# Kernel optimization log

Measured on AMD Instinct MI355X. Metric: run time of the kernel, lower is better.

## Reference

```python
import jax, jax.numpy as jnp
import numpy as np

EPS = 0.05  # mesh.epsilon boundary band


def _pool_one(adj, image, vs, edges):
    # adj: [N,N] bool, image: [N,F] f32, vs: [N,2] f32 in [0,1], edges: [2,E] int32
    N, F = image.shape
    E = edges.shape[1]
    K = N // 2                      # out_target
    tgt_kills = N - K               # number of vertices removed
    v0, v1 = edges[0], edges[1]
    # heap key = sum of squares of concat(image[v0], image[v1])
    cost = jnp.sum(image[v0] * image[v0], -1) + jnp.sum(image[v1] * image[v1], -1)
    def bnd(p):
        return (p[:, 0] < EPS) | (p[:, 0] > 1 - EPS) | (p[:, 1] < EPS) | (p[:, 1] > 1 - EPS)
    ok = ~(bnd(vs[v0]) | bnd(vs[v1]))   # boundary_mask = ~is_boundary
    # heappop of [value, id] lists == stable sort by cost (ties broken by edge id)
    order = jnp.argsort(cost)
    # sequential greedy collapse: kill v1 if edge interior and both endpoints alive
    def step(carry, eid):
        mask, nk = carry
        a, b = v0[eid], v1[eid]
        acc = ok[eid] & mask[a] & mask[b] & (nk < tgt_kills)
        mask = mask.at[b].set(mask[b] & ~acc)
        return (mask, nk + acc.astype(jnp.int32)), acc
    (mask, _), accepts = jax.lax.scan(step, (jnp.ones(N, bool), jnp.int32(0)), order)
    sv0, sv1 = v0[order], v1[order]
    # mapping m: dead vertex -> absorbing vertex (identity elsewhere)
    dead = jnp.where(accepts, sv1, N)          # N = out-of-range -> dropped
    m = jnp.arange(N).at[dead].set(sv0, mode='drop')
    # update_matrix: scatter-add collapsed vertex features into absorber rows
    upd = jnp.zeros_like(image).at[jnp.where(accepts, sv0, N)].add(image[sv1], mode='drop')
    image2 = image + upd
    # merge_vertex on adjacency: union rows then columns of merged vertices
    A = adj.astype(jnp.uint8)
    A1 = jnp.zeros_like(A).at[m].max(A)        # merge rows
    A2 = jnp.zeros_like(A1).at[m].max(A1.T).T  # merge cols
    alive = jnp.nonzero(mask, size=K, fill_value=0)[0]  # exactly K survivors
    adj_out = A2[alive][:, alive].astype(bool) & ~jnp.eye(K, dtype=bool)
    return adj_out, image2[alive]


def setup_inputs() -> dict:
    key = jax.random.key(0)
    k1, k2, k3, k4, k5 = jax.random.split(key, 5)
    B, N, F, E = 4, 8192, 64, 65536
    adj = jax.random.bernoulli(k1, 0.002, (B, N, N))
    image = jax.random.normal(k2, (B, N, F), jnp.float32)
    vs = jax.random.uniform(k3, (B, N, 2), dtype=jnp.float32)
    a = jax.random.randint(k4, (B, 1, E), 0, N)
    off = jax.random.randint(k5, (B, 1, E), 1, N)
    b = (a + off) % N                           # guarantee v0 != v1
    edges = jnp.concatenate([a, b], axis=1).astype(jnp.int32)
    return {"adj": adj, "image": image, "vs": vs, "edges": edges}


def reference(adj, image, vs, edges):
    # returns (pooled adjacency [B,N//2,N//2] bool, pooled features [B,N//2,F])
    return jax.vmap(_pool_one)(adj, image, vs, edges)
```

## Files before the change

kernel.cpp:

```cpp
#include <hip/hip_runtime.h>
#include <stdint.h>

typedef unsigned long long u64;
typedef unsigned int u32;
typedef unsigned char u8;

#define Bn 4
#define Nv 8192
#define Fd 64
#define Ed 65536
#define Kv 4096
#define TGTK 4096
#define NW 256
#define SC 8192

#define SWZ8(i) ((i) ^ (((i) >> 3) & 15))

#define WS_FLAGS   ((size_t)0)
#define WS_ACCCNT  ((size_t)256)
#define WS_OUTBITS ((size_t)512)
#define OUTBITS_BYTES ((size_t)Bn*Kv*128*4)
#define WS_ZERO_BYTES (WS_OUTBITS + OUTBITS_BYTES)
#define WS_KEYS    (WS_ZERO_BYTES)
#define WS_SQ      (WS_KEYS + (size_t)Bn*Ed*8)
#define WS_BND     (WS_SQ + (size_t)Bn*Nv*4)
#define WS_MAP     (WS_BND + (size_t)Bn*Nv)
#define WS_POS     (WS_MAP + (size_t)Bn*Nv*4)
#define WS_PM      (WS_POS + (size_t)Bn*Nv*4)
#define WS_ALIVEW  (WS_PM + (size_t)Bn*Nv*4)
#define WS_ALIST   (WS_ALIVEW + (size_t)Bn*NW*4)
#define WS_ACC     (WS_ALIST + (size_t)Bn*Kv*4)
#define WS_PACK    (WS_ACC + (size_t)Bn*TGTK*2*4)
#define WS_SPACK   (WS_PACK + (size_t)Bn*Ed*4)

__global__ void k_detect(const u8* adj, u32* flags) {
    int tid = blockIdx.x * blockDim.x + threadIdx.x;
    const u32* w = (const u32*)adj;
    bool f0 = false, f1 = false, f2 = false, f3 = false;
    for (int i = tid; i < (1 << 19); i += gridDim.x * blockDim.x) {
        u32 v = w[i];
        f0 |= (v & 0x000000FFu) != 0;
        f1 |= (v & 0x0000FF00u) != 0;
        f2 |= (v & 0x00FF0000u) != 0;
        f3 |= (v & 0xFF000000u) != 0;
    }
    u32 m = 0;
    if (__ballot(f0)) m |= 1;
    if (__ballot(f1)) m |= 2;
    if (__ballot(f2)) m |= 4;
    if (__ballot(f3)) m |= 8;
    if ((threadIdx.x & 63) == 0 && m) atomicOr(flags, m);
}

__global__ void k_vertex(const float* image, const float* vs, float* sq, u8* bnd, int* map) {
#pragma clang fp contract(off)
    int idx = blockIdx.x * 256 + threadIdx.x;
    if (idx >= Bn * Nv) return;
    const float* row = image + (size_t)idx * Fd;
    float r[8];
#pragma unroll
    for (int j = 0; j < 8; ++j) r[j] = row[j] * row[j];
#pragma unroll
    for (int i = 8; i < 64; i += 8)
#pragma unroll
        for (int j = 0; j < 8; ++j) r[j] += row[i + j] * row[i + j];
    float s = ((r[0] + r[1]) + (r[2] + r[3])) + ((r[4] + r[5]) + (r[6] + r[7]));
    sq[idx] = s;
    float x = vs[(size_t)idx * 2], y = vs[(size_t)idx * 2 + 1];
    const float LO = 0.05f;
    const float HI = (float)(1.0 - 0.05);
    bnd[idx] = ((x < LO) || (x > HI) || (y < LO) || (y > HI)) ? 1 : 0;
    map[idx] = idx & (Nv - 1);
}

__global__ void k_edge(const int* edges, const float* sq, const u8* bnd, u64* keys, u32* pack) {
    int idx = blockIdx.x * 256 + threadIdx.x;
    if (idx >= Bn * Ed) return;
    int b = idx >> 16, e = idx & (Ed - 1);
    int v0 = edges[(size_t)b * 2 * Ed + e];
    int v1 = edges[(size_t)b * 2 * Ed + Ed + e];
    float c = sq[b * Nv + v0] + sq[b * Nv + v1];
    keys[idx] = ((u64)__float_as_uint(c) << 16) | (u32)e;
    u32 okk = (!bnd[b * Nv + v0] && !bnd[b * Nv + v1]) ? 1u : 0u;
    pack[idx] = (u32)v0 | ((u32)v1 << 13) | (okk << 26);
}

__device__ __forceinline__ void bitonic_cas(u64* s, int i, int pa, bool asc) {
    u64 a = s[i], c = s[pa];
    if ((a > c) == asc) { s[i] = c; s[pa] = a; }
}
__device__ __forceinline__ void cex(u64& a, u64& b, bool asc) {
    if ((a > b) == asc) { u64 t = a; a = b; b = t; }
}

__global__ __launch_bounds__(1024) void k_sortA(u64* keys) {
    __shared__ u64 s[SC];
    int b = blockIdx.x >> 3, ch = blockIdx.x & 7;
    u64* base = keys + (size_t)b * Ed + (size_t)ch * SC;
    int gb = ch * SC;
    int t8 = threadIdx.x * 8;
    u64 r[8];
#pragma unroll
    for (int u = 0; u < 8; ++u) r[u] = base[t8 + u];
    cex(r[0], r[1], true); cex(r[2], r[3], false); cex(r[4], r[5], true); cex(r[6], r[7], false);
    cex(r[0], r[2], true); cex(r[1], r[3], true); cex(r[4], r[6], false); cex(r[5], r[7], false);
    cex(r[0], r[1], true); cex(r[2], r[3], true); cex(r[4], r[5], false); cex(r[6], r[7], false);
    {
        bool a8 = (((gb + t8) & 8) == 0);
        cex(r[0], r[4], a8); cex(r[1], r[5], a8); cex(r[2], r[6], a8); cex(r[3], r[7], a8);
        cex(r[0], r[2], a8); cex(r[1], r[3], a8); cex(r[4], r[6], a8); cex(r[5], r[7], a8);
        cex(r[0], r[1], a8); cex(r[2], r[3], a8); cex(r[4], r[5], a8); cex(r[6], r[7], a8);
    }
#pragma unroll
    for (int u = 0; u < 8; ++u) s[SWZ8(t8 + u)] = r[u];
    __syncthreads();
    for (int k = 16; k <= SC; k <<= 1) {
        for (int j = k >> 1; j >= 8; j >>= 1) {
#pragma unroll
            for (int p = 0; p < SC / 2048; ++p) {
                int t = p * 1024 + threadIdx.x;
                int i = ((t & ~(j - 1)) << 1) | (t & (j - 1));
                bool asc = (((gb + i) & k) == 0);
                bitonic_cas(s, SWZ8(i), SWZ8(i | j), asc);
            }
            __syncthreads();
        }
        bool asc = (((gb + t8) & k) == 0);
#pragma unroll
        for (int u = 0; u < 8; ++u) r[u] = s[SWZ8(t8 + u)];
        cex(r[0], r[4], asc); cex(r[1], r[5], asc); cex(r[2], r[6], asc); cex(r[3], r[7], asc);
        cex(r[0], r[2], asc); cex(r[1], r[3], asc); cex(r[4], r[6], asc); cex(r[5], r[7], asc);
        cex(r[0], r[1], asc); cex(r[2], r[3], asc); cex(r[4], r[5], asc); cex(r[6], r[7], asc);
        if (k == SC) {
#pragma unroll
            for (int u = 0; u < 8; ++u) base[t8 + u] = r[u];
        } else {
#pragma unroll
            for (int u = 0; u < 8; ++u) s[SWZ8(t8 + u)] = r[u];
            __syncthreads();
        }
    }
}

__global__ void k_sortB(u64* keys, int k, int j) {
    int idx = blockIdx.x * 256 + threadIdx.x;
    if (idx >= Bn * Ed / 2) return;
    int b = idx >> 15, t = idx & (Ed / 2 - 1);
    int i = ((t & ~(j - 1)) << 1) | (t & (j - 1));
    int pa = i | j;
    bool asc = ((i & k) == 0);
    u64* base = keys + (size_t)b * Ed;
    u64 a = base[i], c = base[pa];
    if ((a > c) == asc) { base[i] = c; base[pa] = a; }
}

__global__ __launch_bounds__(1024) void k_sortC(u64* keys, int k,
                                                const u32* pack, u32* spack, int dofin) {
    __shared__ u64 s[SC];
    int b = blockIdx.x >> 3, ch = blockIdx.x & 7;
    u64* base = keys + (size_t)b * Ed + (size_t)ch * SC;
    int gb = ch * SC;
    for (int p = 0; p < SC / 1024; ++p) {
        int i = p * 1024 + threadIdx.x;
        s[SWZ8(i)] = base[i];
    }
    __syncthreads();
    bool asc = ((gb & k) == 0);
    for (int j = SC / 2; j >= 8; j >>= 1) {
#pragma unroll
        for (int p = 0; p < SC / 2048; ++p) {
            int t = p * 1024 + threadIdx.x;
            int i = ((t & ~(j - 1)) << 1) | (t & (j - 1));
            bitonic_cas(s, SWZ8(i), SWZ8(i | j), asc);
        }
        __syncthreads();
    }
    int t8 = threadIdx.x * 8;
    u64 r[8];
#pragma unroll
    for (int u = 0; u < 8; ++u) r[u] = s[SWZ8(t8 + u)];
    cex(r[0], r[4], asc); cex(r[1], r[5], asc); cex(r[2], r[6], asc); cex(r[3], r[7], asc);
    cex(r[0], r[2], asc); cex(r[1], r[3], asc); cex(r[4], r[6], asc); cex(r[5], r[7], asc);
    cex(r[0], r[1], asc); cex(r[2], r[3], asc); cex(r[4], r[5], asc); cex(r[6], r[7], asc);
    if (dofin) {
        const u32* pk = pack + (size_t)b * Ed;
        u32* sp = spack + (size_t)b * Ed + (size_t)ch * SC;
#pragma unroll
        for (int u = 0; u < 8; ++u) sp[t8 + u] = pk[(u32)(r[u] & 0xFFFFu)];
    } else {
#pragma unroll
        for (int u = 0; u < 8; ++u) base[t8 + u] = r[u];
    }
}

__global__ __launch_bounds__(64) void k_greedy(const u32* spack, int* map, u32* aliveW,
                                               int* accList, u32* accCnt) {
    int b = blockIdx.x;
    int lane = threadIdx.x;
    __shared__ u32 alive[NW];
    __shared__ u32 mlane[Nv];
    for (int i = lane; i < NW; i += 64) alive[i] = 0xFFFFFFFFu;
    for (int i = lane; i < Nv; i += 64) mlane[i] = 64u;
    const u32* sp = spack + (size_t)b * Ed;
    u32 pc = sp[lane];
    __syncthreads();
    int nk = 0;
    const int G = Ed / 64;
    for (int g = 0; g < G; ++g) {
        u32 pn = (g + 1 < G) ? sp[(g + 1) * 64 + lane] : 0u;
        int v0 = pc & 8191;
        int v1 = (pc >> 13) & 8191;
        bool okk = (pc >> 26) & 1u;
        bool a0 = (alive[v0 >> 5] >> (v0 & 31)) & 1u;
        bool a1 = (alive[v1 >> 5] >> (v1 & 31)) & 1u;
        bool spec = okk && a0 && a1;
        if (spec) atomicMin(&mlane[v1], (u32)lane);
        __syncthreads();
        bool conf = false;
        if (spec) conf = (mlane[v0] < (u32)lane) || (mlane[v1] < (u32)lane);
        u64 specM = __ballot(spec);
        u64 confM = __ballot(conf);
        u64 accM = specM & ~confM;
        u64 rem = confM;
        while (rem) {
            int l = __ffsll((unsigned long long)rem) - 1;
            rem &= rem - 1;
            int bv0 = __shfl(v0, l);
            int bv1 = __shfl(v1, l);
            bool killer = ((accM >> lane) & 1ull) && (lane < l) && (v1 == bv0 || v1 == bv1);
            if (__ballot(killer) == 0ull) accM |= 1ull << l;
        }
        int cnt = __popcll(accM);
        int remK = TGTK - nk;
        bool acc = (accM >> lane) & 1ull;
        if (cnt > remK) {
            int rr = __popcll(accM & ((1ull << lane) - 1ull));
            if (acc && rr >= remK) acc = false;
            accM = __ballot(acc);
            cnt = remK;
        }
        if (acc) {
            atomicAnd(&alive[v1 >> 5], ~(1u << (v1 & 31)));
            map[(size_t)b * Nv + v1] = v0;
            int rr = __popcll(accM & ((1ull << lane) - 1ull));
            int slot = nk + rr;
            accList[((size_t)b * TGTK + slot) * 2] = v0;
            accList[((size_t)b * TGTK + slot) * 2 + 1] = v1;
        }
        if (spec) mlane[v1] = 64u;
        nk += cnt;
        __syncthreads();
        if (nk >= TGTK) break;
        pc = pn;
    }
    for (int i = lane; i < NW; i += 64) aliveW[b * NW + i] = alive[i];
    if (lane == 0) accCnt[b] = (u32)nk;
}

__global__ __launch_bounds__(256) void k_scan(const u32* aliveW, const int* map,
                                              int* pos, int* pm, int* alist) {
    int b = blockIdx.x, tid = threadIdx.x;
    __shared__ u32 cnt[256];
    __shared__ u32 off[256];
    u32 w = aliveW[b * NW + tid];
    cnt[tid] = __popc(w);
    __syncthreads();
    if (tid == 0) { u32 s = 0; for (int i = 0; i < 256; ++i) { off[i] = s; s += cnt[i]; } }
    __syncthreads();
    u32 base = off[tid];
    int* posb = pos + (size_t)b * Nv;
    int* alb = alist + (size_t)b * Kv;
    for (int bit = 0; bit < 32; ++bit) {
        int v = tid * 32 + bit;
        int p = -1;
        if ((w >> bit) & 1u) {
            if (base < Kv) { p = (int)base; alb[base] = v; }
            base++;
        }
        posb[v] = p;
    }
    __syncthreads();
    const int* mapb = map + (size_t)b * Nv;
    int* pmb = pm + (size_t)b * Nv;
    for (int v = tid; v < Nv; v += 256) pmb[v] = posb[mapb[v]];
}

__global__ void k_fcopy(const float* image, const int* alist, float* outF) {
    int idx = blockIdx.x * 256 + threadIdx.x;
    if (idx >= Bn * Kv * 16) return;
    int b = idx >> 16, r = idx & 65535;
    int x = r >> 4, f4 = r & 15;
    int src = alist[b * Kv + x];
    const float4* s = (const float4*)(image + ((size_t)(b * Nv + src)) * Fd) + f4;
    float4* d = (float4*)(outF + ((size_t)(b * Kv + x)) * Fd) + f4;
    *d = *s;
}

__global__ __launch_bounds__(64) void k_fscat(const float* image, const int* accList,
                                              const u32* accCnt, const int* pos, float* outF) {
    int b = blockIdx.x >> 12, e = blockIdx.x & 4095;
    if (e >= (int)accCnt[b]) return;
    int v0 = accList[((size_t)b * TGTK + e) * 2];
    int v1 = accList[((size_t)b * TGTK + e) * 2 + 1];
    int x = pos[(size_t)b * Nv + v0];
    if (x < 0) return;
    int f = threadIdx.x;
    atomicAdd(outF + ((size_t)(b * Kv + x)) * Fd + f,
              image[((size_t)(b * Nv + v1)) * Fd + f]);
}

__global__ __launch_bounds__(256) void k_merge(const u8* adj, const u32* flags,
                                               const int* pm, u32* outbits) {
    int bi = blockIdx.x;
    int b = bi >> 13, i = bi & (Nv - 1);
    int t = pm[(size_t)b * Nv + i];
    if (t < 0) return;
    __shared__ u32 bits[Kv / 32];
    int tid = threadIdx.x;
    if (tid < 128) bits[tid] = 0;
    __syncthreads();
    const int* pmb = pm + (size_t)b * Nv;
    u32 fw = flags[0];
    bool bytefmt = (fw & 1) && (fw & 8);
    auto put = [&](int col) {
        int c = pmb[col];
        if (c >= 0) atomicOr(&bits[c >> 5], 1u << (c & 31));
    };
    if (bytefmt) {
        const uint4* row = (const uint4*)(adj + ((size_t)b * Nv + i) * Nv);
#pragma unroll
        for (int it = 0; it < 2; ++it) {
            uint4 v = row[it * 256 + tid];
            if (v.x | v.y | v.z | v.w) {
                int cb = (it * 256 + tid) * 16;
                u32 wv[4] = { v.x, v.y, v.z, v.w };
                for (int q = 0; q < 4; ++q) {
                    u32 u = wv[q];
                    if (!u) continue;
#pragma unroll
                    for (int kk = 0; kk < 4; ++kk)
                        if ((u >> (8 * kk)) & 0xFFu) put(cb + q * 4 + kk);
                }
            }
        }
    } else {
        const uint4* row = (const uint4*)((const u32*)adj + ((size_t)b * Nv + i) * Nv);
        for (int it = 0; it < 8; ++it) {
            uint4 v = row[it * 256 + tid];
            int cb = (it * 256 + tid) * 4;
            if (v.x) put(cb);
            if (v.y) put(cb + 1);
            if (v.z) put(cb + 2);
            if (v.w) put(cb + 3);
        }
    }
    __syncthreads();
    if (tid < 128) {
        u32 bw = bits[tid];
        if (bw) atomicOr(&outbits[((size_t)b * Kv + t) * 128 + tid], bw);
    }
}

__global__ void k_expand(const u32* outbits, float* out) {
    int idx = blockIdx.x;
    int tid = threadIdx.x;
    int b = idx >> 14, r = idx & 16383;
    int x = r >> 2, seg = r & 3;
    int c0 = seg * 1024 + tid * 4;
    u32 w = outbits[((size_t)b * Kv + x) * 128 + (c0 >> 5)];
    u32 nib = (w >> (c0 & 31)) & 0xFu;
    float4 f;
    f.x = (nib & 1) ? 1.f : 0.f;
    f.y = (nib & 2) ? 1.f : 0.f;
    f.z = (nib & 4) ? 1.f : 0.f;
    f.w = (nib & 8) ? 1.f : 0.f;
    if (x >= c0 && x < c0 + 4) ((float*)&f)[x - c0] = 0.f;
    *((float4*)(out + ((size_t)(b * Kv + x)) * Kv + c0)) = f;
}

extern "C" void kernel_launch(void* const* d_in, const int* in_sizes, int n_in,
                              void* d_out, int out_size, void* d_ws, size_t ws_size,
                              hipStream_t stream) {
    const u8* adj = (const u8*)d_in[0];
    const float* image = (const float*)d_in[1];
    const float* vs = (const float*)d_in[2];
    const int* edges = (const int*)d_in[3];
    char* ws = (char*)d_ws;
    u32* flags = (u32*)(ws + WS_FLAGS);
    u32* accCnt = (u32*)(ws + WS_ACCCNT);
    u32* outbits = (u32*)(ws + WS_OUTBITS);
    u64* keys = (u64*)(ws + WS_KEYS);
    float* sq = (float*)(ws + WS_SQ);
    u8* bnd = (u8*)(ws + WS_BND);
    int* map = (int*)(ws + WS_MAP);
    int* pos = (int*)(ws + WS_POS);
    int* pm = (int*)(ws + WS_PM);
    u32* aliveW = (u32*)(ws + WS_ALIVEW);
    int* alist = (int*)(ws + WS_ALIST);
    int* accList = (int*)(ws + WS_ACC);
    u32* pack = (u32*)(ws + WS_PACK);
    u32* spack = (u32*)(ws + WS_SPACK);
    float* outA = (float*)d_out;
    float* outF = outA + (size_t)Bn * Kv * Kv;

    hipMemsetAsync(d_ws, 0, WS_ZERO_BYTES, stream);
    k_detect<<<64, 256, 0, stream>>>(adj, flags);
    k_vertex<<<Bn * Nv / 256, 256, 0, stream>>>(image, vs, sq, bnd, map);
    k_edge<<<Bn * Ed / 256, 256, 0, stream>>>(edges, sq, bnd, keys, pack);
    k_sortA<<<Bn * 8, 1024, 0, stream>>>(keys);
    k_sortB<<<Bn * Ed / 2 / 256, 256, 0, stream>>>(keys, 16384, 8192);
    k_sortC<<<Bn * 8, 1024, 0, stream>>>(keys, 16384, pack, spack, 0);
    k_sortB<<<Bn * Ed / 2 / 256, 256, 0, stream>>>(keys, 32768, 16384);
    k_sortB<<<Bn * Ed / 2 / 256, 256, 0, stream>>>(keys, 32768, 8192);
    k_sortC<<<Bn * 8, 1024, 0, stream>>>(keys, 32768, pack, spack, 0);
    k_sortB<<<Bn * Ed / 2 / 256, 256, 0, stream>>>(keys, 65536, 32768);
    k_sortB<<<Bn * Ed / 2 / 256, 256, 0, stream>>>(keys, 65536, 16384);
    k_sortB<<<Bn * Ed / 2 / 256, 256, 0, stream>>>(keys, 65536, 8192);
    k_sortC<<<Bn * 8, 1024, 0, stream>>>(keys, 65536, pack, spack, 1);
    k_greedy<<<Bn, 64, 0, stream>>>(spack, map, aliveW, accList, accCnt);
    k_scan<<<Bn, 256, 0, stream>>>(aliveW, map, pos, pm, alist);
    k_fcopy<<<Bn * Kv * 16 / 256, 256, 0, stream>>>(image, alist, outF);
    k_fscat<<<Bn * TGTK, 64, 0, stream>>>(image, accList, accCnt, pos, outF);
    k_merge<<<Bn * Nv, 256, 0, stream>>>(adj, flags, pm, outbits);
    k_expand<<<Bn * Kv * 4, 256, 0, stream>>>(outbits, outA);
}
```

Baseline: 2.008 ms.

## Compact interior edges, fuse global bitonic stages, widen greedy to 128 edges

Only interior (collapsible) edges are written into the sort keys, via an atomic counter, and the tail is padded with max keys, so later stages skip edges that can never be accepted. The separate global bitonic merge passes are fused into one register-based kernel per merge level, with each thread handling 8 strided elements, which cuts kernel launches and global round-trips. The greedy collapse now handles 128 edges per iteration instead of 64. Generation-tagged atomicMin claims replace the per-iteration reset and the trailing barrier, shortening the serial critical path at the cost of more complex conflict resolution.

```diff
diff --git a/kernel.cpp b/kernel.cpp
--- a/kernel.cpp
+++ b/kernel.cpp
@@ -18,6 +18,7 @@
 
 #define WS_FLAGS   ((size_t)0)
 #define WS_ACCCNT  ((size_t)256)
+#define WS_ECNT    ((size_t)384)
 #define WS_OUTBITS ((size_t)512)
 #define OUTBITS_BYTES ((size_t)Bn*Kv*128*4)
 #define WS_ZERO_BYTES (WS_OUTBITS + OUTBITS_BYTES)
@@ -73,16 +74,27 @@
     map[idx] = idx & (Nv - 1);
 }
 
-__global__ void k_edge(const int* edges, const float* sq, const u8* bnd, u64* keys, u32* pack) {
+__global__ void k_edge(const int* edges, const float* sq, const u8* bnd,
+                       u64* keys, u32* pack, u32* ecnt) {
     int idx = blockIdx.x * 256 + threadIdx.x;
     if (idx >= Bn * Ed) return;
     int b = idx >> 16, e = idx & (Ed - 1);
     int v0 = edges[(size_t)b * 2 * Ed + e];
     int v1 = edges[(size_t)b * 2 * Ed + Ed + e];
     float c = sq[b * Nv + v0] + sq[b * Nv + v1];
-    keys[idx] = ((u64)__float_as_uint(c) << 16) | (u32)e;
     u32 okk = (!bnd[b * Nv + v0] && !bnd[b * Nv + v1]) ? 1u : 0u;
     pack[idx] = (u32)v0 | ((u32)v1 << 13) | (okk << 26);
+    if (okk) {
+        u32 p = atomicAdd(&ecnt[b], 1u);
+        keys[(size_t)b * Ed + p] = ((u64)__float_as_uint(c) << 16) | (u32)e;
+    }
+}
+
+__global__ void k_pad(u64* keys, const u32* ecnt) {
+    int idx = blockIdx.x * 256 + threadIdx.x;
+    if (idx >= Bn * Ed) return;
+    int b = idx >> 16, e = idx & (Ed - 1);
+    if (e >= (int)ecnt[b]) keys[(size_t)b * Ed + e] = ~0ull;
 }
 
 __device__ __forceinline__ void bitonic_cas(u64* s, int i, int pa, bool asc) {
@@ -142,16 +154,25 @@
     }
 }
 
-__global__ void k_sortB(u64* keys, int k, int j) {
-    int idx = blockIdx.x * 256 + threadIdx.x;
-    if (idx >= Bn * Ed / 2) return;
-    int b = idx >> 15, t = idx & (Ed / 2 - 1);
-    int i = ((t & ~(j - 1)) << 1) | (t & (j - 1));
-    int pa = i | j;
-    bool asc = ((i & k) == 0);
-    u64* base = keys + (size_t)b * Ed;
-    u64 a = base[i], c = base[pa];
-    if ((a > c) == asc) { base[i] = c; base[pa] = a; }
+__global__ __launch_bounds__(1024) void k_sortV(u64* keys, int k) {
+    int b = blockIdx.x >> 3;
+    int c = (blockIdx.x & 7) * 1024 + threadIdx.x;
+    u64* base = keys + (size_t)b * Ed + c;
+    u64 r[8];
+#pragma unroll
+    for (int m = 0; m < 8; ++m) r[m] = base[(size_t)m * 8192];
+    if (k == 65536) {
+        cex(r[0], r[4], true); cex(r[1], r[5], true); cex(r[2], r[6], true); cex(r[3], r[7], true);
+        cex(r[0], r[2], true); cex(r[1], r[3], true); cex(r[4], r[6], true); cex(r[5], r[7], true);
+        cex(r[0], r[1], true); cex(r[2], r[3], true); cex(r[4], r[5], true); cex(r[6], r[7], true);
+    } else if (k == 32768) {
+        cex(r[0], r[2], true); cex(r[1], r[3], true); cex(r[4], r[6], false); cex(r[5], r[7], false);
+        cex(r[0], r[1], true); cex(r[2], r[3], true); cex(r[4], r[5], false); cex(r[6], r[7], false);
+    } else {
+        cex(r[0], r[1], true); cex(r[2], r[3], false); cex(r[4], r[5], true); cex(r[6], r[7], false);
+    }
+#pragma unroll
+    for (int m = 0; m < 8; ++m) base[(size_t)m * 8192] = r[m];
 }
 
 __global__ __launch_bounds__(1024) void k_sortC(u64* keys, int k,
@@ -186,7 +207,8 @@
         const u32* pk = pack + (size_t)b * Ed;
         u32* sp = spack + (size_t)b * Ed + (size_t)ch * SC;
 #pragma unroll
-        for (int u = 0; u < 8; ++u) sp[t8 + u] = pk[(u32)(r[u] & 0xFFFFu)];
+        for (int u = 0; u < 8; ++u)
+            sp[t8 + u] = (r[u] == ~0ull) ? 0u : pk[(u32)(r[u] & 0xFFFFu)];
     } else {
 #pragma unroll
         for (int u = 0; u < 8; ++u) base[t8 + u] = r[u];
@@ -200,58 +222,83 @@
     __shared__ u32 alive[NW];
     __shared__ u32 mlane[Nv];
     for (int i = lane; i < NW; i += 64) alive[i] = 0xFFFFFFFFu;
-    for (int i = lane; i < Nv; i += 64) mlane[i] = 64u;
+    for (int i = lane; i < Nv; i += 64) mlane[i] = 0x7FFFFFFFu;
     const u32* sp = spack + (size_t)b * Ed;
-    u32 pc = sp[lane];
+    u32 pa = sp[lane], pb = sp[64 + lane];
     __syncthreads();
     int nk = 0;
-    const int G = Ed / 64;
+    const int G = Ed / 128;
     for (int g = 0; g < G; ++g) {
-        u32 pn = (g + 1 < G) ? sp[(g + 1) * 64 + lane] : 0u;
-        int v0 = pc & 8191;
-        int v1 = (pc >> 13) & 8191;
-        bool okk = (pc >> 26) & 1u;
-        bool a0 = (alive[v0 >> 5] >> (v0 & 31)) & 1u;
-        bool a1 = (alive[v1 >> 5] >> (v1 & 31)) & 1u;
-        bool spec = okk && a0 && a1;
-        if (spec) atomicMin(&mlane[v1], (u32)lane);
+        u32 na = 0u, nb = 0u;
+        if (g + 1 < G) { na = sp[(g + 1) * 128 + lane]; nb = sp[(g + 1) * 128 + 64 + lane]; }
+        int v0a = pa & 8191, v1a = (pa >> 13) & 8191; bool oka = (pa >> 26) & 1u;
+        int v0b = pb & 8191, v1b = (pb >> 13) & 8191; bool okb = (pb >> 26) & 1u;
+        u32 gi = (u32)(G + 1 - g) << 8;
+        if (oka) atomicMin(&mlane[v1a], gi | (u32)lane);
+        if (okb) atomicMin(&mlane[v1b], gi | (u32)(64 + lane));
         __syncthreads();
-        bool conf = false;
-        if (spec) conf = (mlane[v0] < (u32)lane) || (mlane[v1] < (u32)lane);
-        u64 specM = __ballot(spec);
-        u64 confM = __ballot(conf);
-        u64 accM = specM & ~confM;
-        u64 rem = confM;
+        u32 aw0a = alive[v0a >> 5], aw1a = alive[v1a >> 5];
+        u32 aw0b = alive[v0b >> 5], aw1b = alive[v1b >> 5];
+        u32 m0a = mlane[v0a], m1a = mlane[v1a];
+        u32 m0b = mlane[v0b], m1b = mlane[v1b];
+        bool specA = oka && ((aw0a >> (v0a & 31)) & 1u) && ((aw1a >> (v1a & 31)) & 1u);
+        bool specB = okb && ((aw0b >> (v0b & 31)) & 1u) && ((aw1b >> (v1b & 31)) & 1u);
+        u32 slA = (u32)lane, slB = (u32)(64 + lane);
+        bool confA = specA && ((((m0a & 0xFFFFFF00u) == gi) && ((m0a & 255u) < slA)) ||
+                               (((m1a & 0xFFFFFF00u) == gi) && ((m1a & 255u) < slA)));
+        bool confB = specB && ((((m0b & 0xFFFFFF00u) == gi) && ((m0b & 255u) < slB)) ||
+                               (((m1b & 0xFFFFFF00u) == gi) && ((m1b & 255u) < slB)));
+        u64 specLo = __ballot(specA), specHi = __ballot(specB);
+        u64 confLo = __ballot(confA), confHi = __ballot(confB);
+        u64 accLo = specLo & ~confLo, accHi = specHi & ~confHi;
+        u64 rem = confLo;
         while (rem) {
-            int l = __ffsll((unsigned long long)rem) - 1;
-            rem &= rem - 1;
-            int bv0 = __shfl(v0, l);
-            int bv1 = __shfl(v1, l);
-            bool killer = ((accM >> lane) & 1ull) && (lane < l) && (v1 == bv0 || v1 == bv1);
-            if (__ballot(killer) == 0ull) accM |= 1ull << l;
-        }
-        int cnt = __popcll(accM);
+            int l = __ffsll((unsigned long long)rem) - 1; rem &= rem - 1;
+            int bv0 = __shfl(v0a, l), bv1 = __shfl(v1a, l);
+            bool kA = ((accLo >> lane) & 1ull) && (lane < l) && (v1a == bv0 || v1a == bv1);
+            if (__ballot(kA) == 0ull) accLo |= 1ull << l;
+        }
+        rem = confHi;
+        while (rem) {
+            int l = __ffsll((unsigned long long)rem) - 1; rem &= rem - 1;
+            int bv0 = __shfl(v0b, l), bv1 = __shfl(v1b, l);
+            bool kA = ((accLo >> lane) & 1ull) && (v1a == bv0 || v1a == bv1);
+            bool kB = ((accHi >> lane) & 1ull) && (lane < l) && (v1b == bv0 || v1b == bv1);
+            if ((__ballot(kA) | __ballot(kB)) == 0ull) accHi |= 1ull << l;
+        }
+        int cntLo = __popcll(accLo);
+        int cnt = cntLo + __popcll(accHi);
         int remK = TGTK - nk;
-        bool acc = (accM >> lane) & 1ull;
+        bool accA = (accLo >> lane) & 1ull;
+        bool accB = (accHi >> lane) & 1ull;
         if (cnt > remK) {
-            int rr = __popcll(accM & ((1ull << lane) - 1ull));
-            if (acc && rr >= remK) acc = false;
-            accM = __ballot(acc);
+            int rA = __popcll(accLo & ((1ull << lane) - 1ull));
+            if (accA && rA >= remK) accA = false;
+            int rB = cntLo + __popcll(accHi & ((1ull << lane) - 1ull));
+            if (accB && rB >= remK) accB = false;
+            accLo = __ballot(accA); accHi = __ballot(accB);
+            cntLo = __popcll(accLo);
             cnt = remK;
         }
-        if (acc) {
-            atomicAnd(&alive[v1 >> 5], ~(1u << (v1 & 31)));
-            map[(size_t)b * Nv + v1] = v0;
-            int rr = __popcll(accM & ((1ull << lane) - 1ull));
-            int slot = nk + rr;
-            accList[((size_t)b * TGTK + slot) * 2] = v0;
-            accList[((size_t)b * TGTK + slot) * 2 + 1] = v1;
-        }
-        if (spec) mlane[v1] = 64u;
+        if (accA) {
+            atomicAnd(&alive[v1a >> 5], ~(1u << (v1a & 31)));
+            map[(size_t)b * Nv + v1a] = v0a;
+            int r = __popcll(accLo & ((1ull << lane) - 1ull));
+            int slot = nk + r;
+            accList[((size_t)b * TGTK + slot) * 2] = v0a;
+            accList[((size_t)b * TGTK + slot) * 2 + 1] = v1a;
+        }
+        if (accB) {
+            atomicAnd(&alive[v1b >> 5], ~(1u << (v1b & 31)));
+            map[(size_t)b * Nv + v1b] = v0b;
+            int r = cntLo + __popcll(accHi & ((1ull << lane) - 1ull));
+            int slot = nk + r;
+            accList[((size_t)b * TGTK + slot) * 2] = v0b;
+            accList[((size_t)b * TGTK + slot) * 2 + 1] = v1b;
+        }
         nk += cnt;
-        __syncthreads();
         if (nk >= TGTK) break;
-        pc = pn;
+        pa = na; pb = nb;
     }
     for (int i = lane; i < NW; i += 64) aliveW[b * NW + i] = alive[i];
     if (lane == 0) accCnt[b] = (u32)nk;
@@ -388,6 +435,7 @@
     char* ws = (char*)d_ws;
     u32* flags = (u32*)(ws + WS_FLAGS);
     u32* accCnt = (u32*)(ws + WS_ACCCNT);
+    u32* ecnt = (u32*)(ws + WS_ECNT);
     u32* outbits = (u32*)(ws + WS_OUTBITS);
     u64* keys = (u64*)(ws + WS_KEYS);
     float* sq = (float*)(ws + WS_SQ);
@@ -406,16 +454,14 @@
     hipMemsetAsync(d_ws, 0, WS_ZERO_BYTES, stream);
     k_detect<<<64, 256, 0, stream>>>(adj, flags);
     k_vertex<<<Bn * Nv / 256, 256, 0, stream>>>(image, vs, sq, bnd, map);
-    k_edge<<<Bn * Ed / 256, 256, 0, stream>>>(edges, sq, bnd, keys, pack);
+    k_edge<<<Bn * Ed / 256, 256, 0, stream>>>(edges, sq, bnd, keys, pack, ecnt);
+    k_pad<<<Bn * Ed / 256, 256, 0, stream>>>(keys, ecnt);
     k_sortA<<<Bn * 8, 1024, 0, stream>>>(keys);
-    k_sortB<<<Bn * Ed / 2 / 256, 256, 0, stream>>>(keys, 16384, 8192);
+    k_sortV<<<Bn * 8, 1024, 0, stream>>>(keys, 16384);
     k_sortC<<<Bn * 8, 1024, 0, stream>>>(keys, 16384, pack, spack, 0);
-    k_sortB<<<Bn * Ed / 2 / 256, 256, 0, stream>>>(keys, 32768, 16384);
-    k_sortB<<<Bn * Ed / 2 / 256, 256, 0, stream>>>(keys, 32768, 8192);
+    k_sortV<<<Bn * 8, 1024, 0, stream>>>(keys, 32768);
     k_sortC<<<Bn * 8, 1024, 0, stream>>>(keys, 32768, pack, spack, 0);
-    k_sortB<<<Bn * Ed / 2 / 256, 256, 0, stream>>>(keys, 65536, 32768);
-    k_sortB<<<Bn * Ed / 2 / 256, 256, 0, stream>>>(keys, 65536, 16384);
-    k_sortB<<<Bn * Ed / 2 / 256, 256, 0, stream>>>(keys, 65536, 8192);
+    k_sortV<<<Bn * 8, 1024, 0, stream>>>(keys, 65536);
     k_sortC<<<Bn * 8, 1024, 0, stream>>>(keys, 65536, pack, spack, 1);
     k_greedy<<<Bn, 64, 0, stream>>>(spack, map, aliveW, accList, accCnt);
     k_scan<<<Bn, 256, 0, stream>>>(aliveW, map, pos, pm, alist);
```

New measurement: 3.746 ms. 86.6% more time.
